# Kernel tuning notes

Hardware: AMD Instinct MI355X
Metric: run time of the kernel (lower is better)

## Reference

```python
import jax, jax.numpy as jnp
import numpy as np

ALPHA = 0.2  # LeakyReLU negative slope


def setup_inputs() -> dict:
    key = jax.random.key(0)
    k1, k2, k3, k4 = jax.random.split(key, 4)
    N, Fin, Fout = 8192, 256, 64
    inputs = {
        "input": jax.random.normal(k1, (N, Fin), dtype=jnp.float32),
        "adj": jax.random.randint(k2, (N, N), 0, 2, dtype=jnp.int32),
        "W": jax.random.normal(k3, (Fin, Fout), dtype=jnp.float32) * (1.414 * np.sqrt(2.0 / (Fin + Fout))),
        "a": jax.random.normal(k4, (2 * Fout, 1), dtype=jnp.float32) * (1.414 * np.sqrt(2.0 / (2 * Fout + 1))),
    }
    return inputs


def reference(input, adj, W, a):
    # h: [N, Fout]
    h = input @ W
    Fout = h.shape[1]
    # Decompose pairwise score: e[i,j] = leakyrelu(h[i]@a1 + h[j]@a2)
    # (mathematically identical to the original concat+matmul construction,
    #  but avoids the O(N^2 * 2F) intermediate)
    a1, a2 = a[:Fout, 0], a[Fout:, 0]
    s1 = h @ a1  # [N]
    s2 = h @ a2  # [N]
    e = jax.nn.leaky_relu(s1[:, None] + s2[None, :], negative_slope=ALPHA)  # [N, N]
    # Mask non-edges with -10 (as in the original), row softmax
    masked = jnp.where(adj > 0, e, jnp.float32(-10.0))
    attention = jax.nn.softmax(masked, axis=1)
    # dropout p=0.0 (eval/reference mode): identity
    h_prime = attention @ h  # [N, Fout]
    return jax.nn.elu(h_prime)  # concat=True path
```

## Files before the change

### kernel.cpp

```cpp
#include <hip/hip_runtime.h>
#include <hip/hip_bf16.h>
#include <cstdint>
#include <cstddef>

#define NN 8192
#define FIN 256
#define FOUT 64
#define ALPHA_SLOPE 0.2f
#define EXP_M10 4.5399929762484854e-05f

#define JSPLIT 8
#define STRIP 64
#define NSTRIP ((NN / JSPLIT) / STRIP)
#define RB 64
#define WPITCH 144
#define HPITCH 144
#define CP 68

typedef short s16x8 __attribute__((ext_vector_type(8)));
typedef float f32x4 __attribute__((ext_vector_type(4)));
typedef int   i32x4 __attribute__((ext_vector_type(4)));

__device__ __forceinline__ unsigned short f2bf(float x) {
    union { float f; uint32_t u; } v; v.f = x;
    uint32_t u = v.u;
    return (unsigned short)((u + 0x7FFFu + ((u >> 16) & 1u)) >> 16);
}

__device__ __forceinline__ unsigned int rpack2(float a, float b, float& dsum) {
    union { float f; uint32_t u; } va, vb, ra, rb;
    va.f = a; vb.f = b;
    ra.u = (va.u + 0x7FFFu + ((va.u >> 16) & 1u)) & 0xFFFF0000u;
    rb.u = (vb.u + 0x7FFFu + ((vb.u >> 16) & 1u)) & 0xFFFF0000u;
    dsum += ra.f + rb.f;
    return (ra.u >> 16) | rb.u;
}

__device__ __forceinline__ float wval(int a, float s2v, float s1v) {
    float x = s1v + s2v;
    return (a > 0) ? __expf(fmaxf(x, ALPHA_SLOPE * x)) : EXP_M10;
}

__global__ __launch_bounds__(256) void k_h(
    const float* __restrict__ input, const float* __restrict__ W,
    const float* __restrict__ a,
    unsigned short* __restrict__ htg, float* __restrict__ s1, float* __restrict__ s2)
{
    __shared__ __align__(16) unsigned short tile[64][28];
    const int wid  = threadIdx.x >> 6;
    const int lane = threadIdx.x & 63;
    const int i0   = blockIdx.x * 16;
    const int r0   = wid * 4;
    const float* inb = input + (size_t)(i0 + r0) * FIN;

    float acc0 = 0.f, acc1 = 0.f, acc2 = 0.f, acc3 = 0.f;
    #pragma unroll 4
    for (int c = 0; c < FIN; c += 4) {
        float w0 = W[(c + 0) * FOUT + lane];
        float w1 = W[(c + 1) * FOUT + lane];
        float w2 = W[(c + 2) * FOUT + lane];
        float w3 = W[(c + 3) * FOUT + lane];
        float4 x0 = *(const float4*)(inb + 0 * FIN + c);
        float4 x1 = *(const float4*)(inb + 1 * FIN + c);
        float4 x2 = *(const float4*)(inb + 2 * FIN + c);
        float4 x3 = *(const float4*)(inb + 3 * FIN + c);
        acc0 = fmaf(x0.x, w0, fmaf(x0.y, w1, fmaf(x0.z, w2, fmaf(x0.w, w3, acc0))));
        acc1 = fmaf(x1.x, w0, fmaf(x1.y, w1, fmaf(x1.z, w2, fmaf(x1.w, w3, acc1))));
        acc2 = fmaf(x2.x, w0, fmaf(x2.y, w1, fmaf(x2.z, w2, fmaf(x2.w, w3, acc2))));
        acc3 = fmaf(x3.x, w0, fmaf(x3.y, w1, fmaf(x3.z, w2, fmaf(x3.w, w3, acc3))));
    }

    const float a1v = a[lane], a2v = a[FOUT + lane];
    float accs[4] = {acc0, acc1, acc2, acc3};
    #pragma unroll
    for (int r = 0; r < 4; ++r) {
        float v1 = accs[r] * a1v;
        float v2 = accs[r] * a2v;
        #pragma unroll
        for (int off = 32; off; off >>= 1) {
            v1 += __shfl_xor(v1, off);
            v2 += __shfl_xor(v2, off);
        }
        if (lane == 0) { s1[i0 + r0 + r] = v1; s2[i0 + r0 + r] = v2; }
        tile[lane][r0 + r] = f2bf(accs[r]);
    }
    __syncthreads();

    const int feat = threadIdx.x >> 2;
    const int cg   = (threadIdx.x & 3) * 4;
    uint2 q = *(const uint2*)&tile[feat][cg];
    *(uint2*)(htg + (size_t)feat * NN + i0 + cg) = q;
}

__global__ __launch_bounds__(512, 8) void k_attn(
    const int* __restrict__ adj,
    const unsigned short* __restrict__ htg,
    const float* __restrict__ s1g, const float* __restrict__ s2g,
    float* __restrict__ slabs)
{
    __shared__ __align__(16) unsigned char wbuf[2][RB * WPITCH];
    __shared__ __align__(16) unsigned char hbuf[2][64 * HPITCH];

    const int t    = threadIdx.x;
    const int wid  = t >> 6;
    const int lane = t & 63;
    const int bi   = blockIdx.x >> 3;
    const int js   = blockIdx.x & 7;
    const int i0   = bi * RB;
    const int jbase = js * (NN / JSPLIT);
    const int m    = lane & 15;
    const int quad = lane >> 4;
    const int rg   = wid >> 1;
    const int fg   = wid & 1;

    const int srow = t >> 3;
    const int scol = (t & 7) * 8;
    const float s1v = s1g[i0 + srow];

    f32x4 acc0 = {0,0,0,0}, acc1 = {0,0,0,0};
    float dsum = 0.f;

    const int* adjrow = adj + (size_t)(i0 + srow) * NN + jbase;
    const unsigned short* hrow = htg + (size_t)srow * NN + jbase;
    const float* s2p = s2g + jbase;

    {
        i32x4  a0 = *(const i32x4*)(adjrow + scol);
        i32x4  a1 = *(const i32x4*)(adjrow + scol + 4);
        float4 v0 = *(const float4*)(s2p + scol);
        float4 v1 = *(const float4*)(s2p + scol + 4);
        s16x8  h0 = *(const s16x8*)(hrow + scol);
        uint4 q;
        q.x = rpack2(wval(a0.x, v0.x, s1v), wval(a0.y, v0.y, s1v), dsum);
        q.y = rpack2(wval(a0.z, v0.z, s1v), wval(a0.w, v0.w, s1v), dsum);
        q.z = rpack2(wval(a1.x, v1.x, s1v), wval(a1.y, v1.y, s1v), dsum);
        q.w = rpack2(wval(a1.z, v1.z, s1v), wval(a1.w, v1.w, s1v), dsum);
        *(uint4*)&wbuf[0][srow * WPITCH + (t & 7) * 16] = q;
        *(s16x8*)&hbuf[0][srow * HPITCH + (t & 7) * 16] = h0;
    }
    __syncthreads();

    for (int s = 0; s < NSTRIP; ++s) {
        const int cur = s & 1, nxt = cur ^ 1;
        const bool more = (s + 1 < NSTRIP);

        i32x4 a0, a1; float4 v0, v1; s16x8 h0;
        if (more) {
            const int jn = (s + 1) * STRIP;
            a0 = *(const i32x4*)(adjrow + jn + scol);
            a1 = *(const i32x4*)(adjrow + jn + scol + 4);
            v0 = *(const float4*)(s2p + jn + scol);
            v1 = *(const float4*)(s2p + jn + scol + 4);
            h0 = *(const s16x8*)(hrow + jn + scol);
        }

        #pragma unroll
        for (int kk = 0; kk < 2; ++kk) {
            const int cb = kk * 64 + quad * 16;
            s16x8 af = *(const s16x8*)&wbuf[cur][(rg * 16 + m) * WPITCH + cb];
            s16x8 b0 = *(const s16x8*)&hbuf[cur][(fg * 32 + m) * HPITCH + cb];
            s16x8 b1 = *(const s16x8*)&hbuf[cur][(fg * 32 + 16 + m) * HPITCH + cb];
            acc0 = __builtin_amdgcn_mfma_f32_16x16x32_bf16(af, b0, acc0, 0, 0, 0);
            acc1 = __builtin_amdgcn_mfma_f32_16x16x32_bf16(af, b1, acc1, 0, 0, 0);
        }

        if (more) {
            uint4 q;
            q.x = rpack2(wval(a0.x, v0.x, s1v), wval(a0.y, v0.y, s1v), dsum);
            q.y = rpack2(wval(a0.z, v0.z, s1v), wval(a0.w, v0.w, s1v), dsum);
            q.z = rpack2(wval(a1.x, v1.x, s1v), wval(a1.y, v1.y, s1v), dsum);
            q.w = rpack2(wval(a1.z, v1.z, s1v), wval(a1.w, v1.w, s1v), dsum);
            *(uint4*)&wbuf[nxt][srow * WPITCH + (t & 7) * 16] = q;
            *(s16x8*)&hbuf[nxt][srow * HPITCH + (t & 7) * 16] = h0;
        }
        __syncthreads();
    }

    float* slab = slabs + (size_t)js * ((size_t)NN * CP);
    const int r0 = i0 + rg * 16 + quad * 4;
    #pragma unroll
    for (int reg = 0; reg < 4; ++reg) {
        size_t ro = (size_t)(r0 + reg) * CP;
        slab[ro + fg * 32 + m]      = acc0[reg];
        slab[ro + fg * 32 + 16 + m] = acc1[reg];
    }
    dsum += __shfl_xor(dsum, 1);
    dsum += __shfl_xor(dsum, 2);
    dsum += __shfl_xor(dsum, 4);
    if ((t & 7) == 0) slab[(size_t)(i0 + srow) * CP + 64] = dsum;
}

__global__ __launch_bounds__(256) void k_norm(
    const float* __restrict__ slabs, float* __restrict__ out)
{
    int gid = blockIdx.x * 256 + threadIdx.x;
    int i = gid >> 6, k = gid & 63;
    float num = 0.f, den = 0.f;
    #pragma unroll
    for (int js = 0; js < JSPLIT; ++js) {
        const float* row = slabs + (size_t)js * ((size_t)NN * CP) + (size_t)i * CP;
        num += row[k];
        den += row[64];
    }
    float v = num / den;
    out[gid] = (v > 0.f) ? v : (__expf(v) - 1.f);
}

extern "C" void kernel_launch(void* const* d_in, const int* in_sizes, int n_in,
                              void* d_out, int out_size, void* d_ws, size_t ws_size,
                              hipStream_t stream) {
    const float* input = (const float*)d_in[0];
    const int*   adj   = (const int*)d_in[1];
    const float* W     = (const float*)d_in[2];
    const float* a     = (const float*)d_in[3];
    float* out = (float*)d_out;

    char* ws = (char*)d_ws;
    float* slabs = (float*)ws;
    size_t off = (size_t)JSPLIT * NN * CP * sizeof(float);
    unsigned short* htg = (unsigned short*)(ws + off);
    off += (size_t)FOUT * NN * sizeof(unsigned short);
    float* s1 = (float*)(ws + off); off += NN * sizeof(float);
    float* s2 = (float*)(ws + off);

    k_h   <<<NN / 16, 256, 0, stream>>>(input, W, a, htg, s1, s2);
    k_attn<<<(NN / RB) * JSPLIT, 512, 0, stream>>>(adj, htg, s1, s2, slabs);
    k_norm<<<NN * FOUT / 256, 256, 0, stream>>>(slabs, out);
}
```

Measured before the change: 413.3 us.

## Double strip width, halve j-split, and stage s2 in shared memory

The attention kernel now processes 128-column strips instead of 64 and splits the j range 4 ways instead of 8. Each thread issues more loads per iteration, and there are half as many barriers per column processed. The block's s2 slice is preloaded into LDS once, so the inner loop no longer reads it from global memory. Shared memory use grows to roughly 78KB per block, and the occupancy hint drops from 8 to 4, which costs latency hiding. With only 512 blocks the grid is also smaller.

```diff
diff --git a/kernel.cpp b/kernel.cpp
--- a/kernel.cpp
+++ b/kernel.cpp
@@ -9,12 +9,13 @@
 #define ALPHA_SLOPE 0.2f
 #define EXP_M10 4.5399929762484854e-05f
 
-#define JSPLIT 8
-#define STRIP 64
-#define NSTRIP ((NN / JSPLIT) / STRIP)
+#define JSPLIT 4
+#define JRANGE (NN / JSPLIT)
+#define STRIP 128
+#define NSTRIP (JRANGE / STRIP)
 #define RB 64
-#define WPITCH 144
-#define HPITCH 144
+#define WPITCH 272
+#define HPITCH 272
 #define CP 68
 
 typedef short s16x8 __attribute__((ext_vector_type(8)));
@@ -92,7 +93,7 @@
     *(uint2*)(htg + (size_t)feat * NN + i0 + cg) = q;
 }
 
-__global__ __launch_bounds__(512, 8) void k_attn(
+__global__ __launch_bounds__(512, 4) void k_attn(
     const int* __restrict__ adj,
     const unsigned short* __restrict__ htg,
     const float* __restrict__ s1g, const float* __restrict__ s2g,
@@ -100,43 +101,59 @@
 {
     __shared__ __align__(16) unsigned char wbuf[2][RB * WPITCH];
     __shared__ __align__(16) unsigned char hbuf[2][64 * HPITCH];
+    __shared__ __align__(16) float s2buf[JRANGE];
 
     const int t    = threadIdx.x;
     const int wid  = t >> 6;
     const int lane = t & 63;
-    const int bi   = blockIdx.x >> 3;
-    const int js   = blockIdx.x & 7;
+    const int bi   = blockIdx.x >> 2;
+    const int js   = blockIdx.x & 3;
     const int i0   = bi * RB;
-    const int jbase = js * (NN / JSPLIT);
+    const int jbase = js * JRANGE;
     const int m    = lane & 15;
     const int quad = lane >> 4;
     const int rg   = wid >> 1;
     const int fg   = wid & 1;
 
     const int srow = t >> 3;
-    const int scol = (t & 7) * 8;
+    const int scol = (t & 7) * 16;
     const float s1v = s1g[i0 + srow];
 
     f32x4 acc0 = {0,0,0,0}, acc1 = {0,0,0,0};
     float dsum = 0.f;
 
-    const int* adjrow = adj + (size_t)(i0 + srow) * NN + jbase;
-    const unsigned short* hrow = htg + (size_t)srow * NN + jbase;
-    const float* s2p = s2g + jbase;
+    const int* adjrow = adj + (size_t)(i0 + srow) * NN + jbase + scol;
+    const unsigned short* hrow = htg + (size_t)srow * NN + jbase + scol;
 
     {
-        i32x4  a0 = *(const i32x4*)(adjrow + scol);
-        i32x4  a1 = *(const i32x4*)(adjrow + scol + 4);
-        float4 v0 = *(const float4*)(s2p + scol);
-        float4 v1 = *(const float4*)(s2p + scol + 4);
-        s16x8  h0 = *(const s16x8*)(hrow + scol);
-        uint4 q;
-        q.x = rpack2(wval(a0.x, v0.x, s1v), wval(a0.y, v0.y, s1v), dsum);
-        q.y = rpack2(wval(a0.z, v0.z, s1v), wval(a0.w, v0.w, s1v), dsum);
-        q.z = rpack2(wval(a1.x, v1.x, s1v), wval(a1.y, v1.y, s1v), dsum);
-        q.w = rpack2(wval(a1.z, v1.z, s1v), wval(a1.w, v1.w, s1v), dsum);
-        *(uint4*)&wbuf[0][srow * WPITCH + (t & 7) * 16] = q;
-        *(s16x8*)&hbuf[0][srow * HPITCH + (t & 7) * 16] = h0;
+        *(float4*)&s2buf[t * 4] = *(const float4*)(s2g + jbase + t * 4);
+
+        i32x4  a0 = *(const i32x4*)(adjrow);
+        i32x4  a1 = *(const i32x4*)(adjrow + 4);
+        i32x4  a2 = *(const i32x4*)(adjrow + 8);
+        i32x4  a3 = *(const i32x4*)(adjrow + 12);
+        float4 v0 = *(const float4*)(s2g + jbase + scol);
+        float4 v1 = *(const float4*)(s2g + jbase + scol + 4);
+        float4 v2 = *(const float4*)(s2g + jbase + scol + 8);
+        float4 v3 = *(const float4*)(s2g + jbase + scol + 12);
+        s16x8  h0 = *(const s16x8*)(hrow);
+        s16x8  h1 = *(const s16x8*)(hrow + 8);
+
+        uint4 q0, q1;
+        q0.x = rpack2(wval(a0.x, v0.x, s1v), wval(a0.y, v0.y, s1v), dsum);
+        q0.y = rpack2(wval(a0.z, v0.z, s1v), wval(a0.w, v0.w, s1v), dsum);
+        q0.z = rpack2(wval(a1.x, v1.x, s1v), wval(a1.y, v1.y, s1v), dsum);
+        q0.w = rpack2(wval(a1.z, v1.z, s1v), wval(a1.w, v1.w, s1v), dsum);
+        q1.x = rpack2(wval(a2.x, v2.x, s1v), wval(a2.y, v2.y, s1v), dsum);
+        q1.y = rpack2(wval(a2.z, v2.z, s1v), wval(a2.w, v2.w, s1v), dsum);
+        q1.z = rpack2(wval(a3.x, v3.x, s1v), wval(a3.y, v3.y, s1v), dsum);
+        q1.w = rpack2(wval(a3.z, v3.z, s1v), wval(a3.w, v3.w, s1v), dsum);
+        unsigned char* wd = &wbuf[0][srow * WPITCH + scol * 2];
+        *(uint4*)(wd)      = q0;
+        *(uint4*)(wd + 16) = q1;
+        unsigned char* hd = &hbuf[0][srow * HPITCH + scol * 2];
+        *(s16x8*)(hd)      = h0;
+        *(s16x8*)(hd + 16) = h1;
     }
     __syncthreads();
 
@@ -144,18 +161,19 @@
         const int cur = s & 1, nxt = cur ^ 1;
         const bool more = (s + 1 < NSTRIP);
 
-        i32x4 a0, a1; float4 v0, v1; s16x8 h0;
+        i32x4 a0, a1, a2, a3; s16x8 h0, h1;
         if (more) {
             const int jn = (s + 1) * STRIP;
-            a0 = *(const i32x4*)(adjrow + jn + scol);
-            a1 = *(const i32x4*)(adjrow + jn + scol + 4);
-            v0 = *(const float4*)(s2p + jn + scol);
-            v1 = *(const float4*)(s2p + jn + scol + 4);
-            h0 = *(const s16x8*)(hrow + jn + scol);
+            a0 = *(const i32x4*)(adjrow + jn);
+            a1 = *(const i32x4*)(adjrow + jn + 4);
+            a2 = *(const i32x4*)(adjrow + jn + 8);
+            a3 = *(const i32x4*)(adjrow + jn + 12);
+            h0 = *(const s16x8*)(hrow + jn);
+            h1 = *(const s16x8*)(hrow + jn + 8);
         }
 
         #pragma unroll
-        for (int kk = 0; kk < 2; ++kk) {
+        for (int kk = 0; kk < 4; ++kk) {
             const int cb = kk * 64 + quad * 16;
             s16x8 af = *(const s16x8*)&wbuf[cur][(rg * 16 + m) * WPITCH + cb];
             s16x8 b0 = *(const s16x8*)&hbuf[cur][(fg * 32 + m) * HPITCH + cb];
@@ -165,13 +183,26 @@
         }
 
         if (more) {
-            uint4 q;
-            q.x = rpack2(wval(a0.x, v0.x, s1v), wval(a0.y, v0.y, s1v), dsum);
-            q.y = rpack2(wval(a0.z, v0.z, s1v), wval(a0.w, v0.w, s1v), dsum);
-            q.z = rpack2(wval(a1.x, v1.x, s1v), wval(a1.y, v1.y, s1v), dsum);
-            q.w = rpack2(wval(a1.z, v1.z, s1v), wval(a1.w, v1.w, s1v), dsum);
-            *(uint4*)&wbuf[nxt][srow * WPITCH + (t & 7) * 16] = q;
-            *(s16x8*)&hbuf[nxt][srow * HPITCH + (t & 7) * 16] = h0;
+            const int jn = (s + 1) * STRIP;
+            float4 v0 = *(const float4*)&s2buf[jn + scol];
+            float4 v1 = *(const float4*)&s2buf[jn + scol + 4];
+            float4 v2 = *(const float4*)&s2buf[jn + scol + 8];
+            float4 v3 = *(const float4*)&s2buf[jn + scol + 12];
+            uint4 q0, q1;
+            q0.x = rpack2(wval(a0.x, v0.x, s1v), wval(a0.y, v0.y, s1v), dsum);
+            q0.y = rpack2(wval(a0.z, v0.z, s1v), wval(a0.w, v0.w, s1v), dsum);
+            q0.z = rpack2(wval(a1.x, v1.x, s1v), wval(a1.y, v1.y, s1v), dsum);
+            q0.w = rpack2(wval(a1.z, v1.z, s1v), wval(a1.w, v1.w, s1v), dsum);
+            q1.x = rpack2(wval(a2.x, v2.x, s1v), wval(a2.y, v2.y, s1v), dsum);
+            q1.y = rpack2(wval(a2.z, v2.z, s1v), wval(a2.w, v2.w, s1v), dsum);
+            q1.z = rpack2(wval(a3.x, v3.x, s1v), wval(a3.y, v3.y, s1v), dsum);
+            q1.w = rpack2(wval(a3.z, v3.z, s1v), wval(a3.w, v3.w, s1v), dsum);
+            unsigned char* wd = &wbuf[nxt][srow * WPITCH + scol * 2];
+            *(uint4*)(wd)      = q0;
+            *(uint4*)(wd + 16) = q1;
+            unsigned char* hd = &hbuf[nxt][srow * HPITCH + scol * 2];
+            *(s16x8*)(hd)      = h0;
+            *(s16x8*)(hd + 16) = h1;
         }
         __syncthreads();
     }
```

After: 395.9 us. 4.2% less time.
